# Performance work log

Measured on AMD Instinct MI355X. Metric: run time of the kernel, lower is better.

The kernel has to match this reference:

```python
import jax, jax.numpy as jnp
import numpy as np

N = 100000      # total nodes across batch of graphs
E = 1600000     # total edges (avg degree 16)
DIN = 16        # raw node feature dim
H = 128         # social_hidden_dim
HEADS = 4
DOUT = H // HEADS
LAYERS = 2
G = 64          # number of graphs in batch
FOUT = 256      # fusion_hidden_dim
NEG_SLOPE = 0.2


def layer_norm(x, g, b, eps=1e-5):
    mu = x.mean(-1, keepdims=True)
    var = ((x - mu) ** 2).mean(-1, keepdims=True)
    return (x - mu) / jnp.sqrt(var + eps) * g + b


def gat_conv(h, src, dst, W, a_src, a_dst, bias):
    # h: [N,H]; src/dst: [E+N] (self-loops included)
    hp = (h @ W).reshape(N, HEADS, DOUT)                    # [N,heads,dout]
    al_s = jnp.einsum('nhd,hd->nh', hp, a_src)              # [N,heads]
    al_d = jnp.einsum('nhd,hd->nh', hp, a_dst)
    logits = jax.nn.leaky_relu(al_s[src] + al_d[dst], NEG_SLOPE)  # [Etot,heads]
    m = jax.ops.segment_max(logits, dst, num_segments=N)    # segment softmax over dst
    e = jnp.exp(logits - m[dst])
    denom = jax.ops.segment_sum(e, dst, num_segments=N)
    alpha = e / (denom[dst] + 1e-16)                        # [Etot,heads]
    msg = hp[src] * alpha[:, :, None]                       # [Etot,heads,dout]
    out = jax.ops.segment_sum(msg, dst, num_segments=N)     # scatter-add
    return out.reshape(N, H) + bias


def setup_inputs():
    key = jax.random.key(0)
    ks = jax.random.split(key, 24)
    s = 0.05
    inp = {
        'x': jax.random.normal(ks[0], (N, DIN), jnp.float32),
        'edge_index': jax.random.randint(ks[1], (2, E), 0, N, jnp.int32),
        'node2graph': (jnp.arange(N, dtype=jnp.int32) * G // N).astype(jnp.int32),
        'Wp': jax.random.normal(ks[2], (DIN, H)) * s,
        'bp': jnp.zeros((H,)),
        'Wq1': jax.random.normal(ks[3], (2 * H, H)) * s,
        'bq1': jnp.zeros((H,)),
        'gq': jnp.ones((H,)), 'beq': jnp.zeros((H,)),
        'Wq2': jax.random.normal(ks[4], (H, FOUT)) * s,
        'bq2': jnp.zeros((FOUT,)),
    }
    for i in range(LAYERS):
        inp[f'Wg{i}'] = jax.random.normal(ks[5 + 4 * i], (H, H)) * s
        inp[f'as{i}'] = jax.random.normal(ks[6 + 4 * i], (HEADS, DOUT)) * s
        inp[f'ad{i}'] = jax.random.normal(ks[7 + 4 * i], (HEADS, DOUT)) * s
        inp[f'bg{i}'] = jnp.zeros((H,))
        inp[f'g{i}'] = jnp.ones((H,))
        inp[f'be{i}'] = jnp.zeros((H,))
    return inp


def reference(x, edge_index, node2graph, Wp, bp, Wq1, bq1, gq, beq, Wq2, bq2,
              Wg0, as0, ad0, bg0, g0, be0, Wg1, as1, ad1, bg1, g1, be1):
    loop = jnp.arange(N, dtype=edge_index.dtype)
    src = jnp.concatenate([edge_index[0], loop])  # add self-loops (PyG default)
    dst = jnp.concatenate([edge_index[1], loop])

    h = jax.nn.gelu(x @ Wp + bp, approximate=False)
    params = [(Wg0, as0, ad0, bg0, g0, be0), (Wg1, as1, ad1, bg1, g1, be1)]
    for (W, a_s, a_d, b, g, be) in params:
        h_new = gat_conv(h, src, dst, W, a_s, a_d, b)
        h = layer_norm(h_new + h, g, be)  # dims match -> residual

    counts = jax.ops.segment_sum(jnp.ones((N, 1), h.dtype), node2graph, num_segments=G)
    mean_pool = jax.ops.segment_sum(h, node2graph, num_segments=G) / jnp.maximum(counts, 1.0)
    max_pool = jax.ops.segment_max(h, node2graph, num_segments=G)
    emb = jnp.concatenate([mean_pool, max_pool], axis=-1)  # [G, 2H]

    p = layer_norm(emb @ Wq1 + bq1, gq, beq)
    p = jax.nn.gelu(p, approximate=False)
    return p @ Wq2 + bq2  # [G, FOUT]
```

## Files before the change

kernel.cpp:

```cpp
#include <hip/hip_runtime.h>

typedef unsigned short u16;
typedef unsigned char u8;
typedef unsigned int u32;
typedef unsigned long long u64;
typedef short short8 __attribute__((ext_vector_type(8)));
typedef float f32x4 __attribute__((ext_vector_type(4)));
typedef float f32x2 __attribute__((ext_vector_type(2)));

#define NN   100000
#define EE   1600000
#define ETOT (EE + NN)
#define NG   64
#define WSTR 136
#define SCANB 98
#define NB   98
#define BCAP 24576
#define OCAP 262144
#define EPB  4096

constexpr size_t AL256(size_t x) { return (x + 255) & ~(size_t)255; }
constexpr size_t OFF_FLAG   = 0;
constexpr size_t OFF_BSUM   = AL256(OFF_FLAG + 256);
constexpr size_t OFF_BCNT   = AL256(OFF_BSUM + 128 * 4);
constexpr size_t OFF_ROWPTR = AL256(OFF_BCNT + 128 * 4);
constexpr size_t OFF_DEG    = AL256(OFF_ROWPTR + (size_t)(NN + 1) * 4);
constexpr size_t OFF_COL    = AL256(OFF_DEG + (size_t)NN * 4);
constexpr size_t OFF_ALS    = AL256(OFF_COL + (size_t)ETOT * 4);
constexpr size_t OFF_ALD    = AL256(OFF_ALS + (size_t)NN * 4 * 4);
constexpr size_t OFF_GSUM   = AL256(OFF_ALD + (size_t)NN * 4 * 4);
constexpr size_t OFF_GKEY   = AL256(OFF_GSUM + (size_t)NG * 128 * 4);
constexpr size_t OFF_GCNT   = AL256(OFF_GKEY + (size_t)NG * 128 * 4);
constexpr size_t OFF_H      = AL256(OFF_GCNT + (size_t)NG * 4);
constexpr size_t OFF_HPB    = AL256(OFF_H + (size_t)NN * 128 * 2);
constexpr size_t OFF_EBUF   = AL256(OFF_HPB + (size_t)NN * 128 * 1);
constexpr size_t OFF_OBUF   = AL256(OFF_EBUF + (size_t)NB * BCAP * 8);
constexpr size_t WS_TOTAL   = AL256(OFF_OBUF + (size_t)OCAP * 8);

__device__ u64 g_ws[WS_TOTAL / 8];

__device__ __forceinline__ char* wsp() { return (char*)g_ws; }
#define WS_FLAG   ((int*)(wsp() + OFF_FLAG))
#define WS_BSUM   ((int*)(wsp() + OFF_BSUM))
#define WS_BCNT   ((int*)(wsp() + OFF_BCNT))
#define WS_ROWPTR ((int*)(wsp() + OFF_ROWPTR))
#define WS_DEG    ((int*)(wsp() + OFF_DEG))
#define WS_COL    ((int*)(wsp() + OFF_COL))
#define WS_ALS    ((float*)(wsp() + OFF_ALS))
#define WS_ALD    ((float*)(wsp() + OFF_ALD))
#define WS_GSUM   ((float*)(wsp() + OFF_GSUM))
#define WS_GKEY   ((u32*)(wsp() + OFF_GKEY))
#define WS_GCNT   ((int*)(wsp() + OFF_GCNT))
#define WS_H      ((u16*)(wsp() + OFF_H))
#define WS_HPB    ((u8*)(wsp() + OFF_HPB))
#define WS_EBUF   ((u64*)(wsp() + OFF_EBUF))
#define WS_OBUF   ((u64*)(wsp() + OFF_OBUF))

__device__ __forceinline__ float b2f(u16 u) { return __uint_as_float(((u32)u) << 16); }
__device__ __forceinline__ float b2f_lo(u32 u) { return __uint_as_float(u << 16); }
__device__ __forceinline__ float b2f_hi(u32 u) { return __uint_as_float(u & 0xffff0000u); }
__device__ __forceinline__ u16 f2bf(float f) {
    u32 u = __float_as_uint(f);
    return (u16)((u + 0x7fffu + ((u >> 16) & 1u)) >> 16);
}
__device__ __forceinline__ float ldf(const void* p, int i, int bf) {
    return bf ? b2f(((const u16*)p)[i]) : ((const float*)p)[i];
}
__device__ __forceinline__ int ldint(const int* p, long long i, int wide) {
    return wide ? p[i * 2] : p[(size_t)i];
}
__device__ __forceinline__ u32 fkey(float f) {
    u32 u = __float_as_uint(f);
    return (u >> 31) ? ~u : (u | 0x80000000u);
}
__device__ __forceinline__ float funkey(u32 k) {
    u32 u = (k & 0x80000000u) ? (k & 0x7fffffffu) : ~k;
    return __uint_as_float(u);
}

__global__ __launch_bounds__(256) void k_zero(const void* __restrict__ x,
                                              const int* __restrict__ ei) {
    if (blockIdx.x == 0 && threadIdx.x < 64) {
        int t = threadIdx.x;
        const u16* p = (const u16*)x;
        u16 u = p[t * 2];
        int e = (u >> 7) & 0xff;
        int ok = ((u & 0x7fffu) == 0) || (e >= 0x60 && e <= 0x9f);
        u64 m1 = __ballot(ok);
        int z = (ei[t * 2 + 1] == 0);
        u64 m2 = __ballot(z);
        if (t == 0) {
            WS_FLAG[0] = (__popcll(m1) >= 48) ? 1 : 0;
            WS_FLAG[1] = (__popcll(m2) >= 56) ? 1 : 0;
        }
    }
    if (blockIdx.x == 0 && threadIdx.x == 64) WS_FLAG[2] = 0;
    int i = blockIdx.x * 256 + threadIdx.x;
    if (i < NN) WS_DEG[i] = 0;
    if (i < NG * 128) { WS_GSUM[i] = 0.f; WS_GKEY[i] = 0u; }
    if (i < NG) WS_GCNT[i] = 0;
    if (i < NB) WS_BCNT[i] = 0;
}

__global__ __launch_bounds__(256) void k_bucket(const int* __restrict__ ei) {
    __shared__ int lcnt[NB], lbase[NB], lcur[NB];
    int t = threadIdx.x;
    int wide = WS_FLAG[1];
    for (int i = t; i < NB; i += 256) { lcnt[i] = 0; lcur[i] = 0; }
    __syncthreads();
    int e0 = blockIdx.x * EPB + t;
    int sA[16], dA[16];
#pragma unroll
    for (int j = 0; j < 16; j++) {
        int e = e0 + j * 256;
        int s = -1, d = 0;
        if (e < ETOT) {
            if (e < EE) {
                if (wide) { s = ((const int2*)ei)[e].x; d = ((const int2*)ei)[(size_t)EE + e].x; }
                else      { s = ei[e];                  d = ei[(size_t)EE + e]; }
            } else { s = e - EE; d = s; }
            if ((u32)s >= NN || (u32)d >= NN) s = -1;
        }
        sA[j] = s; dA[j] = d;
        if (s >= 0) atomicAdd(&lcnt[d >> 10], 1);
    }
    __syncthreads();
    for (int i = t; i < NB; i += 256)
        lbase[i] = atomicAdd(&WS_BCNT[i], lcnt[i]);
    __syncthreads();
    u64* ebuf = WS_EBUF;
#pragma unroll
    for (int j = 0; j < 16; j++) {
        int s = sA[j], d = dA[j];
        if (s < 0) continue;
        int b = d >> 10;
        int r = atomicAdd(&lcur[b], 1);
        int slot = lbase[b] + r;
        u64 pk = ((u64)(u32)d << 32) | (u32)s;
        if (slot < BCAP) {
            ebuf[(size_t)b * BCAP + slot] = pk;
        } else {
            int o = atomicAdd(&WS_FLAG[2], 1);
            if (o < OCAP) {
                WS_OBUF[o] = pk;
                atomicAdd(&WS_DEG[d], 1);
            }
        }
    }
}

__global__ __launch_bounds__(1024) void k_scan1() {
    __shared__ int sdat[1024];
    __shared__ int hist[1024];
    int b = blockIdx.x, t = threadIdx.x;
    hist[t] = 0;
    __syncthreads();
    int bc = WS_BCNT[b]; if (bc > BCAP) bc = BCAP;
    const u64* eb = WS_EBUF + (size_t)b * BCAP;
    for (int i = t; i < bc; i += 1024) {
        int d = (int)(eb[i] >> 32);
        atomicAdd(&hist[d & 1023], 1);
    }
    __syncthreads();
    int i = b * 1024 + t;
    int v = (i < NN) ? (WS_DEG[i] + hist[t]) : 0;
    sdat[t] = v;
    __syncthreads();
    for (int off = 1; off < 1024; off <<= 1) {
        int u = 0;
        if (t >= off) u = sdat[t - off];
        __syncthreads();
        if (t >= off) sdat[t] += u;
        __syncthreads();
    }
    if (i < NN) WS_ROWPTR[i] = sdat[t] - v;
    if (t == 1023) WS_BSUM[b] = sdat[1023];
}

__global__ __launch_bounds__(256) void k_place() {
    __shared__ int cur[1024];
    __shared__ int sb[128];
    int b = blockIdx.x, t = threadIdx.x;
    if (t < 128) sb[t] = (t < SCANB) ? WS_BSUM[t] : 0;
    __syncthreads();
    for (int off = 1; off < 128; off <<= 1) {
        int u = 0;
        if (t < 128 && t >= off) u = sb[t - off];
        __syncthreads();
        if (t < 128 && t >= off) sb[t] += u;
        __syncthreads();
    }
    int add = (b > 0) ? sb[b - 1] : 0;
    int n0 = b << 10;
    for (int i = t; i < 1024; i += 256) {
        int n = n0 + i;
        int r = 0;
        if (n < NN) {
            r = WS_ROWPTR[n] + add;
            WS_ROWPTR[n] = r;
        }
        cur[i] = r;
    }
    if (b == 0 && t == 0) WS_ROWPTR[NN] = sb[127];
    __syncthreads();
    int bc = WS_BCNT[b]; if (bc > BCAP) bc = BCAP;
    const u64* eb = WS_EBUF + (size_t)b * BCAP;
    for (int i = t; i < bc; i += 256) {
        u64 pk = eb[i];
        int d = (int)(pk >> 32), s = (int)(pk & 0xffffffffu);
        int pos = atomicAdd(&cur[d & 1023], 1);
        WS_COL[pos] = s;
    }
    int cnt = WS_FLAG[2]; if (cnt > OCAP) cnt = OCAP;
    for (int i = t; i < cnt; i += 256) {
        u64 pk = WS_OBUF[i];
        int d = (int)(pk >> 32);
        if ((d >> 10) == b) {
            int pos = atomicAdd(&cur[d & 1023], 1);
            WS_COL[pos] = (int)(pk & 0xffffffffu);
        }
    }
}

__global__ __launch_bounds__(128) void k_proj(const void* __restrict__ x,
                                              const void* __restrict__ Wp,
                                              const void* __restrict__ bp) {
    __shared__ float sW[16 * 128];
    int t = threadIdx.x;
    int bf = WS_FLAG[0];
    for (int i = t; i < 16 * 128; i += 128) sW[i] = ldf(Wp, i, bf);
    __syncthreads();
    float bj = ldf(bp, t, bf);
    for (int n = blockIdx.x; n < NN; n += gridDim.x) {
        float acc = bj;
#pragma unroll
        for (int k = 0; k < 16; k++)
            acc = fmaf(ldf(x, n * 16 + k, bf), sW[k * 128 + t], acc);
        float g = 0.5f * acc * (1.0f + erff(acc * 0.70710678118654752f));
        WS_H[(size_t)n * 128 + t] = f2bf(g);
    }
}

__global__ __launch_bounds__(256) void k_gemm(const void* __restrict__ Wg,
                                              const void* __restrict__ a_s,
                                              const void* __restrict__ a_d) {
    __shared__ __align__(16) u16 sWt[128 * WSTR];
    __shared__ __align__(16) u16 sH[16 * WSTR];
    int t = threadIdx.x;
    int bf = WS_FLAG[0];
    for (int idx = t; idx < 128 * 128; idx += 256) {
        int k = idx >> 7, n = idx & 127;
        sWt[n * WSTR + k] = bf ? ((const u16*)Wg)[idx] : f2bf(((const float*)Wg)[idx]);
    }
    __syncthreads();
    int wv = t >> 6, lane = t & 63;
    int n0 = wv * 32;
    int quad = lane >> 4, m16 = lane & 15;
    float as0v = ldf(a_s, n0 + m16, bf),      as1v = ldf(a_s, n0 + 16 + m16, bf);
    float ad0v = ldf(a_d, n0 + m16, bf),      ad1v = ldf(a_d, n0 + 16 + m16, bf);
    short8 bfr[2][4];
#pragma unroll
    for (int nt = 0; nt < 2; nt++) {
        int n = n0 + nt * 16 + m16;
#pragma unroll
        for (int ks = 0; ks < 4; ks++)
            bfr[nt][ks] = *(const short8*)&sWt[n * WSTR + ks * 32 + quad * 8];
    }
    u8* hp = WS_HPB;
    const u32* h32 = (const u32*)WS_H;
    u32* sH32 = (u32*)sH;
    for (int m0 = blockIdx.x * 16; m0 < NN; m0 += gridDim.x * 16) {
        __syncthreads();
        for (int idx = t; idx < 16 * 64; idx += 256) {
            int r = idx >> 6, c2 = idx & 63;
            sH32[r * 68 + c2] = h32[(size_t)(m0 + r) * 64 + c2];
        }
        __syncthreads();
        f32x4 acc0 = {0.f, 0.f, 0.f, 0.f};
        f32x4 acc1 = {0.f, 0.f, 0.f, 0.f};
#pragma unroll
        for (int ks = 0; ks < 4; ks++) {
            short8 af = *(const short8*)&sH[m16 * WSTR + ks * 32 + quad * 8];
            acc0 = __builtin_amdgcn_mfma_f32_16x16x32_bf16(af, bfr[0][ks], acc0, 0, 0, 0);
            acc1 = __builtin_amdgcn_mfma_f32_16x16x32_bf16(af, bfr[1][ks], acc1, 0, 0, 0);
        }
#pragma unroll
        for (int r = 0; r < 4; r++) {
            size_t row = (size_t)(m0 + quad * 4 + r) * 128;
            u32 pk8 = (u32)__builtin_amdgcn_cvt_pk_fp8_f32(acc0[r], acc1[r], 0, false);
            hp[row + n0 + m16]      = (u8)(pk8 & 0xff);
            hp[row + n0 + 16 + m16] = (u8)((pk8 >> 8) & 0xff);
            float ps = acc0[r] * as0v + acc1[r] * as1v;
            float pd = acc0[r] * ad0v + acc1[r] * ad1v;
#pragma unroll
            for (int m = 1; m <= 8; m <<= 1) {
                ps += __shfl_xor(ps, m);
                pd += __shfl_xor(pd, m);
            }
            if (m16 == 0) {
                int nrow = m0 + quad * 4 + r;
                WS_ALS[nrow * 4 + wv] = ps;
                WS_ALD[nrow * 4 + wv] = pd;
            }
        }
    }
}

__global__ __launch_bounds__(512) void k_gat(const void* __restrict__ bg,
                                             const void* __restrict__ gam,
                                             const void* __restrict__ bet) {
    int wid = threadIdx.x >> 6, lane = threadIdx.x & 63;
    int n = blockIdx.x * 8 + wid;
    if (n >= NN) return;
    int bf = WS_FLAG[0];
    const int* col = WS_COL;
    const float* als = WS_ALS;
    int k0 = WS_ROWPTR[n], deg = WS_ROWPTR[n + 1] - k0;
    int hd = lane >> 4, eo = lane & 15;
    float aldh = WS_ALD[n * 4 + hd];
    const u16* hp16 = (const u16*)WS_HPB;
    u32* h32 = (u32*)WS_H;
    u32 hv = h32[(size_t)n * 64 + lane];
    int base48 = lane & 48;

    int i0 = eo, i1 = eo + 16;
    int e0 = k0 + (i0 < deg ? i0 : 0);
    int e1 = k0 + (i1 < deg ? i1 : 0);
    int sc0 = col[e0];
    int sc1 = col[e1];
    float v0 = als[sc0 * 4 + hd] + aldh;
    float v1 = als[sc1 * 4 + hd] + aldh;
    v0 = v0 > 0.f ? v0 : 0.2f * v0;
    v1 = v1 > 0.f ? v1 : 0.2f * v1;
    float w0 = (i0 < deg) ? __expf(v0) : 0.f;
    float w1 = (i1 < deg) ? __expf(v1) : 0.f;
    float se = w0 + w1;
    float a0 = 0.f, a1 = 0.f;

#pragma unroll
    for (int j = 0; j < 16; j++) {
        float wj = __shfl(w0, base48 + j);
        int   sj = __builtin_amdgcn_readlane(sc0, j);
        u16 pv = hp16[(size_t)sj * 64 + lane];
        f32x2 mv = __builtin_amdgcn_cvt_pk_f32_fp8((int)pv, false);
        a0 = fmaf(wj, mv.x, a0);
        a1 = fmaf(wj, mv.y, a1);
    }
#pragma unroll
    for (int j = 0; j < 16; j++) {
        float wj = __shfl(w1, base48 + j);
        int   sj = __builtin_amdgcn_readlane(sc1, j);
        u16 pv = hp16[(size_t)sj * 64 + lane];
        f32x2 mv = __builtin_amdgcn_cvt_pk_f32_fp8((int)pv, false);
        a0 = fmaf(wj, mv.x, a0);
        a1 = fmaf(wj, mv.y, a1);
    }

    if (__builtin_expect(deg > 32, 0)) {
        for (int c = 32; c < deg; c += 16) {
            int i = c + eo;
            float w = 0.f; int scol = 0;
            if (i < deg) {
                scol = col[k0 + i];
                float v = als[scol * 4 + hd] + aldh;
                v = v > 0.f ? v : 0.2f * v;
                w = __expf(v);
            }
            se += w;
            int rem = deg - c; if (rem > 16) rem = 16;
            for (int j = 0; j < rem; j++) {
                float wj = __shfl(w, base48 + j);
                int sj = __shfl(scol, base48 + j);
                u16 pv = hp16[(size_t)sj * 64 + lane];
                f32x2 mv = __builtin_amdgcn_cvt_pk_f32_fp8((int)pv, false);
                a0 = fmaf(wj, mv.x, a0);
                a1 = fmaf(wj, mv.y, a1);
            }
        }
    }

    se += __shfl_xor(se, 1);
    se += __shfl_xor(se, 2);
    se += __shfl_xor(se, 4);
    se += __shfl_xor(se, 8);
    float inv = 1.f / (se + 1e-16f);
    int d0 = lane * 2, d1 = d0 + 1;
    float r0 = a0 * inv + ldf(bg, d0, bf) + b2f_lo(hv);
    float r1 = a1 * inv + ldf(bg, d1, bf) + b2f_hi(hv);
    float s1 = r0 + r1;
#pragma unroll
    for (int m = 1; m <= 32; m <<= 1) s1 += __shfl_xor(s1, m);
    float mu = s1 * (1.f / 128.f);
    float e0f = r0 - mu, e1f = r1 - mu;
    float s2 = e0f * e0f + e1f * e1f;
#pragma unroll
    for (int m = 1; m <= 32; m <<= 1) s2 += __shfl_xor(s2, m);
    float rstd = rsqrtf(s2 * (1.f / 128.f) + 1e-5f);
    float y0 = e0f * rstd * ldf(gam, d0, bf) + ldf(bet, d0, bf);
    float y1 = e1f * rstd * ldf(gam, d1, bf) + ldf(bet, d1, bf);
    h32[(size_t)n * 64 + lane] = (u32)f2bf(y0) | ((u32)f2bf(y1) << 16);
}

__global__ __launch_bounds__(128) void k_pool(const int* __restrict__ n2g) {
    int j = threadIdx.x;
    int wide = WS_FLAG[1];
    int n0 = blockIdx.x * 128;
    int n1 = n0 + 128; if (n1 > NN) n1 = NN;
    float runs = 0.f, runm = -3.4e38f;
    int rung = -1, runc = 0;
    for (int n = n0; n < n1; n++) {
        int g = ldint(n2g, n, wide);
        if (g != rung) {
            if (rung >= 0 && (u32)rung < NG) {
                atomicAdd(&WS_GSUM[rung * 128 + j], runs);
                atomicMax(&WS_GKEY[rung * 128 + j], fkey(runm));
                if (j == 0) atomicAdd(&WS_GCNT[rung], runc);
            }
            rung = g; runs = 0.f; runm = -3.4e38f; runc = 0;
        }
        float v = b2f(WS_H[(size_t)n * 128 + j]);
        runs += v;
        runm = fmaxf(runm, v);
        runc++;
    }
    if (rung >= 0 && (u32)rung < NG) {
        atomicAdd(&WS_GSUM[rung * 128 + j], runs);
        atomicMax(&WS_GKEY[rung * 128 + j], fkey(runm));
        if (j == 0) atomicAdd(&WS_GCNT[rung], runc);
    }
}

__global__ __launch_bounds__(256) void k_head(const void* __restrict__ Wq1,
                                              const void* __restrict__ bq1,
                                              const void* __restrict__ gq,
                                              const void* __restrict__ beq,
                                              const void* __restrict__ Wq2,
                                              const void* __restrict__ bq2,
                                              float* __restrict__ out) {
    __shared__ float sem[256];
    __shared__ float sp[128];
    __shared__ float red[4];
    int g = blockIdx.x, t = threadIdx.x;
    int bf = WS_FLAG[0];
    float cnt = fmaxf((float)WS_GCNT[g], 1.f);
    if (t < 128) sem[t] = WS_GSUM[g * 128 + t] / cnt;
    else         sem[t] = funkey(WS_GKEY[g * 128 + (t - 128)]);
    __syncthreads();
    float a = 0.f;
    if (t < 128) {
        a = ldf(bq1, t, bf);
        for (int k = 0; k < 256; k++) a = fmaf(sem[k], ldf(Wq1, k * 128 + t, bf), a);
    }
    int lane = t & 63, wv = t >> 6;
    float s1 = (t < 128) ? a : 0.f;
#pragma unroll
    for (int m = 1; m <= 32; m <<= 1) s1 += __shfl_xor(s1, m);
    if (lane == 0) red[wv] = s1;
    __syncthreads();
    float mu = (red[0] + red[1]) * (1.f / 128.f);
    float d = (t < 128) ? (a - mu) : 0.f;
    float s2 = d * d;
#pragma unroll
    for (int m = 1; m <= 32; m <<= 1) s2 += __shfl_xor(s2, m);
    __syncthreads();
    if (lane == 0) red[wv] = s2;
    __syncthreads();
    float var = (red[0] + red[1]) * (1.f / 128.f);
    if (t < 128) {
        float p = d * rsqrtf(var + 1e-5f) * ldf(gq, t, bf) + ldf(beq, t, bf);
        sp[t] = 0.5f * p * (1.0f + erff(p * 0.70710678118654752f));
    }
    __syncthreads();
    float o = ldf(bq2, t, bf);
    for (int k = 0; k < 128; k++)
        o = fmaf(sp[k], ldf(Wq2, k * 256 + t, bf), o);
    out[g * 256 + t] = o;
}

extern "C" void kernel_launch(void* const* d_in, const int* in_sizes, int n_in,
                              void* d_out, int out_size, void* d_ws, size_t ws_size,
                              hipStream_t stream) {
    const void* x   = d_in[0];
    const int* ei   = (const int*)d_in[1];
    const int* n2g  = (const int*)d_in[2];
    const void* Wp  = d_in[3];
    const void* bp  = d_in[4];
    const void* Wq1 = d_in[5];
    const void* bq1 = d_in[6];
    const void* gq  = d_in[7];
    const void* beq = d_in[8];
    const void* Wq2 = d_in[9];
    const void* bq2 = d_in[10];
    const void* Wg0 = d_in[11];
    const void* as0 = d_in[12];
    const void* ad0 = d_in[13];
    const void* bg0 = d_in[14];
    const void* g0  = d_in[15];
    const void* be0 = d_in[16];
    const void* Wg1 = d_in[17];
    const void* as1 = d_in[18];
    const void* ad1 = d_in[19];
    const void* bg1 = d_in[20];
    const void* g1  = d_in[21];
    const void* be1 = d_in[22];
    (void)d_ws; (void)ws_size; (void)in_sizes; (void)n_in; (void)out_size;

    k_zero<<<(NN + 255) / 256, 256, 0, stream>>>(x, ei);

    k_bucket<<<(ETOT + EPB - 1) / EPB, 256, 0, stream>>>(ei);
    k_scan1<<<SCANB, 1024, 0, stream>>>();
    k_place<<<NB, 256, 0, stream>>>();

    k_proj<<<2048, 128, 0, stream>>>(x, Wp, bp);

    k_gemm<<<1024, 256, 0, stream>>>(Wg0, as0, ad0);
    k_gat<<<(NN + 7) / 8, 512, 0, stream>>>(bg0, g0, be0);
    k_gemm<<<1024, 256, 0, stream>>>(Wg1, as1, ad1);
    k_gat<<<(NN + 7) / 8, 512, 0, stream>>>(bg1, g1, be1);

    k_pool<<<(NN + 127) / 128, 128, 0, stream>>>(n2g);
    k_head<<<NG, 256, 0, stream>>>(Wq1, bq1, gq, beq, Wq2, bq2, (float*)d_out);
}
```

Baseline: 562.2 us.

## Replace bucketed CSR build with atomic count/fill and split GAT edges across half-waves

The CSR construction drops the bucketed edge buffer and overflow path in favor of a direct per-node atomic degree count, a two-pass scan, and a second pass that atomically fills column indices. The GAT aggregation now has each half-wavefront process a different edge with 4 fp8 features per lane via 32-bit loads, combining the halves with a cross-lane add. It also loops generically over degree in chunks of 32 instead of using a fixed 32-edge fast path plus a slow tail. The CSR change removes large intermediate buffer traffic but adds heavy global atomics on node degrees and a second read of the edge list. Column order within a row becomes nondeterministic.

```diff
diff --git a/kernel.cpp b/kernel.cpp
--- a/kernel.cpp
+++ b/kernel.cpp
@@ -14,16 +14,12 @@
 #define NG   64
 #define WSTR 136
 #define SCANB 98
-#define NB   98
-#define BCAP 24576
-#define OCAP 262144
 #define EPB  4096
 
 constexpr size_t AL256(size_t x) { return (x + 255) & ~(size_t)255; }
 constexpr size_t OFF_FLAG   = 0;
 constexpr size_t OFF_BSUM   = AL256(OFF_FLAG + 256);
-constexpr size_t OFF_BCNT   = AL256(OFF_BSUM + 128 * 4);
-constexpr size_t OFF_ROWPTR = AL256(OFF_BCNT + 128 * 4);
+constexpr size_t OFF_ROWPTR = AL256(OFF_BSUM + 128 * 4);
 constexpr size_t OFF_DEG    = AL256(OFF_ROWPTR + (size_t)(NN + 1) * 4);
 constexpr size_t OFF_COL    = AL256(OFF_DEG + (size_t)NN * 4);
 constexpr size_t OFF_ALS    = AL256(OFF_COL + (size_t)ETOT * 4);
@@ -33,16 +29,13 @@
 constexpr size_t OFF_GCNT   = AL256(OFF_GKEY + (size_t)NG * 128 * 4);
 constexpr size_t OFF_H      = AL256(OFF_GCNT + (size_t)NG * 4);
 constexpr size_t OFF_HPB    = AL256(OFF_H + (size_t)NN * 128 * 2);
-constexpr size_t OFF_EBUF   = AL256(OFF_HPB + (size_t)NN * 128 * 1);
-constexpr size_t OFF_OBUF   = AL256(OFF_EBUF + (size_t)NB * BCAP * 8);
-constexpr size_t WS_TOTAL   = AL256(OFF_OBUF + (size_t)OCAP * 8);
+constexpr size_t WS_TOTAL   = AL256(OFF_HPB + (size_t)NN * 128 * 1);
 
 __device__ u64 g_ws[WS_TOTAL / 8];
 
 __device__ __forceinline__ char* wsp() { return (char*)g_ws; }
 #define WS_FLAG   ((int*)(wsp() + OFF_FLAG))
 #define WS_BSUM   ((int*)(wsp() + OFF_BSUM))
-#define WS_BCNT   ((int*)(wsp() + OFF_BCNT))
 #define WS_ROWPTR ((int*)(wsp() + OFF_ROWPTR))
 #define WS_DEG    ((int*)(wsp() + OFF_DEG))
 #define WS_COL    ((int*)(wsp() + OFF_COL))
@@ -53,8 +46,6 @@
 #define WS_GCNT   ((int*)(wsp() + OFF_GCNT))
 #define WS_H      ((u16*)(wsp() + OFF_H))
 #define WS_HPB    ((u8*)(wsp() + OFF_HPB))
-#define WS_EBUF   ((u64*)(wsp() + OFF_EBUF))
-#define WS_OBUF   ((u64*)(wsp() + OFF_OBUF))
 
 __device__ __forceinline__ float b2f(u16 u) { return __uint_as_float(((u32)u) << 16); }
 __device__ __forceinline__ float b2f_lo(u32 u) { return __uint_as_float(u << 16); }
@@ -94,76 +85,35 @@
             WS_FLAG[1] = (__popcll(m2) >= 56) ? 1 : 0;
         }
     }
-    if (blockIdx.x == 0 && threadIdx.x == 64) WS_FLAG[2] = 0;
     int i = blockIdx.x * 256 + threadIdx.x;
     if (i < NN) WS_DEG[i] = 0;
     if (i < NG * 128) { WS_GSUM[i] = 0.f; WS_GKEY[i] = 0u; }
     if (i < NG) WS_GCNT[i] = 0;
-    if (i < NB) WS_BCNT[i] = 0;
-}
-
-__global__ __launch_bounds__(256) void k_bucket(const int* __restrict__ ei) {
-    __shared__ int lcnt[NB], lbase[NB], lcur[NB];
-    int t = threadIdx.x;
+}
+
+__global__ __launch_bounds__(256) void k_deg(const int* __restrict__ ei) {
     int wide = WS_FLAG[1];
-    for (int i = t; i < NB; i += 256) { lcnt[i] = 0; lcur[i] = 0; }
-    __syncthreads();
-    int e0 = blockIdx.x * EPB + t;
-    int sA[16], dA[16];
+    int e0 = blockIdx.x * EPB + threadIdx.x;
 #pragma unroll
     for (int j = 0; j < 16; j++) {
         int e = e0 + j * 256;
-        int s = -1, d = 0;
         if (e < ETOT) {
+            int s, d;
             if (e < EE) {
                 if (wide) { s = ((const int2*)ei)[e].x; d = ((const int2*)ei)[(size_t)EE + e].x; }
                 else      { s = ei[e];                  d = ei[(size_t)EE + e]; }
             } else { s = e - EE; d = s; }
-            if ((u32)s >= NN || (u32)d >= NN) s = -1;
-        }
-        sA[j] = s; dA[j] = d;
-        if (s >= 0) atomicAdd(&lcnt[d >> 10], 1);
-    }
-    __syncthreads();
-    for (int i = t; i < NB; i += 256)
-        lbase[i] = atomicAdd(&WS_BCNT[i], lcnt[i]);
-    __syncthreads();
-    u64* ebuf = WS_EBUF;
-#pragma unroll
-    for (int j = 0; j < 16; j++) {
-        int s = sA[j], d = dA[j];
-        if (s < 0) continue;
-        int b = d >> 10;
-        int r = atomicAdd(&lcur[b], 1);
-        int slot = lbase[b] + r;
-        u64 pk = ((u64)(u32)d << 32) | (u32)s;
-        if (slot < BCAP) {
-            ebuf[(size_t)b * BCAP + slot] = pk;
-        } else {
-            int o = atomicAdd(&WS_FLAG[2], 1);
-            if (o < OCAP) {
-                WS_OBUF[o] = pk;
-                atomicAdd(&WS_DEG[d], 1);
-            }
+            if ((u32)s < NN && (u32)d < NN) atomicAdd(&WS_DEG[d], 1);
         }
     }
 }
 
 __global__ __launch_bounds__(1024) void k_scan1() {
     __shared__ int sdat[1024];
-    __shared__ int hist[1024];
     int b = blockIdx.x, t = threadIdx.x;
-    hist[t] = 0;
-    __syncthreads();
-    int bc = WS_BCNT[b]; if (bc > BCAP) bc = BCAP;
-    const u64* eb = WS_EBUF + (size_t)b * BCAP;
-    for (int i = t; i < bc; i += 1024) {
-        int d = (int)(eb[i] >> 32);
-        atomicAdd(&hist[d & 1023], 1);
-    }
-    __syncthreads();
     int i = b * 1024 + t;
-    int v = (i < NN) ? (WS_DEG[i] + hist[t]) : 0;
+    int v = 0;
+    if (i < NN) { v = WS_DEG[i]; WS_DEG[i] = 0; }
     sdat[t] = v;
     __syncthreads();
     for (int off = 1; off < 1024; off <<= 1) {
@@ -173,12 +123,11 @@
         if (t >= off) sdat[t] += u;
         __syncthreads();
     }
-    if (i < NN) WS_ROWPTR[i] = sdat[t] - v;
+    if (i <= NN) WS_ROWPTR[i] = sdat[t] - v;
     if (t == 1023) WS_BSUM[b] = sdat[1023];
 }
 
-__global__ __launch_bounds__(256) void k_place() {
-    __shared__ int cur[1024];
+__global__ __launch_bounds__(1024) void k_fin() {
     __shared__ int sb[128];
     int b = blockIdx.x, t = threadIdx.x;
     if (t < 128) sb[t] = (t < SCANB) ? WS_BSUM[t] : 0;
@@ -190,34 +139,29 @@
         if (t < 128 && t >= off) sb[t] += u;
         __syncthreads();
     }
-    int add = (b > 0) ? sb[b - 1] : 0;
-    int n0 = b << 10;
-    for (int i = t; i < 1024; i += 256) {
-        int n = n0 + i;
-        int r = 0;
-        if (n < NN) {
-            r = WS_ROWPTR[n] + add;
-            WS_ROWPTR[n] = r;
-        }
-        cur[i] = r;
-    }
-    if (b == 0 && t == 0) WS_ROWPTR[NN] = sb[127];
-    __syncthreads();
-    int bc = WS_BCNT[b]; if (bc > BCAP) bc = BCAP;
-    const u64* eb = WS_EBUF + (size_t)b * BCAP;
-    for (int i = t; i < bc; i += 256) {
-        u64 pk = eb[i];
-        int d = (int)(pk >> 32), s = (int)(pk & 0xffffffffu);
-        int pos = atomicAdd(&cur[d & 1023], 1);
-        WS_COL[pos] = s;
-    }
-    int cnt = WS_FLAG[2]; if (cnt > OCAP) cnt = OCAP;
-    for (int i = t; i < cnt; i += 256) {
-        u64 pk = WS_OBUF[i];
-        int d = (int)(pk >> 32);
-        if ((d >> 10) == b) {
-            int pos = atomicAdd(&cur[d & 1023], 1);
-            WS_COL[pos] = (int)(pk & 0xffffffffu);
+    if (b > 0) {
+        int add = sb[b - 1];
+        int i = b * 1024 + t;
+        if (i <= NN) WS_ROWPTR[i] += add;
+    }
+}
+
+__global__ __launch_bounds__(256) void k_fill(const int* __restrict__ ei) {
+    int wide = WS_FLAG[1];
+    int e0 = blockIdx.x * EPB + threadIdx.x;
+#pragma unroll
+    for (int j = 0; j < 16; j++) {
+        int e = e0 + j * 256;
+        if (e < ETOT) {
+            int s, d;
+            if (e < EE) {
+                if (wide) { s = ((const int2*)ei)[e].x; d = ((const int2*)ei)[(size_t)EE + e].x; }
+                else      { s = ei[e];                  d = ei[(size_t)EE + e]; }
+            } else { s = e - EE; d = s; }
+            if ((u32)s < NN && (u32)d < NN) {
+                int pos = WS_ROWPTR[d] + atomicAdd(&WS_DEG[d], 1);
+                WS_COL[pos] = s;
+            }
         }
     }
 }
@@ -317,88 +261,88 @@
     const float* als = WS_ALS;
     int k0 = WS_ROWPTR[n], deg = WS_ROWPTR[n + 1] - k0;
     int hd = lane >> 4, eo = lane & 15;
+    int half = lane >> 5, q = lane & 31, hq = q >> 3;
     float aldh = WS_ALD[n * 4 + hd];
-    const u16* hp16 = (const u16*)WS_HPB;
-    u32* h32 = (u32*)WS_H;
-    u32 hv = h32[(size_t)n * 64 + lane];
-    int base48 = lane & 48;
-
-    int i0 = eo, i1 = eo + 16;
-    int e0 = k0 + (i0 < deg ? i0 : 0);
-    int e1 = k0 + (i1 < deg ? i1 : 0);
-    int sc0 = col[e0];
-    int sc1 = col[e1];
-    float v0 = als[sc0 * 4 + hd] + aldh;
-    float v1 = als[sc1 * 4 + hd] + aldh;
-    v0 = v0 > 0.f ? v0 : 0.2f * v0;
-    v1 = v1 > 0.f ? v1 : 0.2f * v1;
-    float w0 = (i0 < deg) ? __expf(v0) : 0.f;
-    float w1 = (i1 < deg) ? __expf(v1) : 0.f;
-    float se = w0 + w1;
-    float a0 = 0.f, a1 = 0.f;
-
-#pragma unroll
-    for (int j = 0; j < 16; j++) {
-        float wj = __shfl(w0, base48 + j);
-        int   sj = __builtin_amdgcn_readlane(sc0, j);
-        u16 pv = hp16[(size_t)sj * 64 + lane];
-        f32x2 mv = __builtin_amdgcn_cvt_pk_f32_fp8((int)pv, false);
-        a0 = fmaf(wj, mv.x, a0);
-        a1 = fmaf(wj, mv.y, a1);
-    }
-#pragma unroll
-    for (int j = 0; j < 16; j++) {
-        float wj = __shfl(w1, base48 + j);
-        int   sj = __builtin_amdgcn_readlane(sc1, j);
-        u16 pv = hp16[(size_t)sj * 64 + lane];
-        f32x2 mv = __builtin_amdgcn_cvt_pk_f32_fp8((int)pv, false);
-        a0 = fmaf(wj, mv.x, a0);
-        a1 = fmaf(wj, mv.y, a1);
-    }
-
-    if (__builtin_expect(deg > 32, 0)) {
-        for (int c = 32; c < deg; c += 16) {
-            int i = c + eo;
-            float w = 0.f; int scol = 0;
-            if (i < deg) {
-                scol = col[k0 + i];
-                float v = als[scol * 4 + hd] + aldh;
-                v = v > 0.f ? v : 0.2f * v;
-                w = __expf(v);
+    const u32* hp32 = (const u32*)WS_HPB;
+    const u64* h64 = (const u64*)WS_H;
+    u64 hv = h64[(size_t)n * 32 + q];
+    float se = 0.f, a0 = 0.f, a1 = 0.f, a2 = 0.f, a3 = 0.f;
+    int wsel = hq * 16 + half;
+
+    for (int c = 0; c < deg; c += 32) {
+        int i0 = c + eo, i1 = c + 16 + eo;
+        int e0 = k0 + (i0 < deg ? i0 : 0);
+        int e1 = k0 + (i1 < deg ? i1 : 0);
+        int sc0 = col[e0];
+        int sc1 = col[e1];
+        float v0 = als[sc0 * 4 + hd] + aldh;
+        float v1 = als[sc1 * 4 + hd] + aldh;
+        v0 = v0 > 0.f ? v0 : 0.2f * v0;
+        v1 = v1 > 0.f ? v1 : 0.2f * v1;
+        float w0 = (i0 < deg) ? __expf(v0) : 0.f;
+        float w1 = (i1 < deg) ? __expf(v1) : 0.f;
+        se += w0 + w1;
+#pragma unroll
+        for (int j = 0; j < 8; j++) {
+            float wj = __shfl(w0, wsel + 2 * j);
+            int   sj = __shfl(sc0, half + 2 * j);
+            u32 v = hp32[(size_t)sj * 32 + q];
+            f32x2 mlo = __builtin_amdgcn_cvt_pk_f32_fp8((int)v, false);
+            f32x2 mhi = __builtin_amdgcn_cvt_pk_f32_fp8((int)v, true);
+            a0 = fmaf(wj, mlo.x, a0);
+            a1 = fmaf(wj, mlo.y, a1);
+            a2 = fmaf(wj, mhi.x, a2);
+            a3 = fmaf(wj, mhi.y, a3);
+        }
+        if (deg > c + 16) {
+#pragma unroll
+            for (int j = 0; j < 8; j++) {
+                float wj = __shfl(w1, wsel + 2 * j);
+                int   sj = __shfl(sc1, half + 2 * j);
+                u32 v = hp32[(size_t)sj * 32 + q];
+                f32x2 mlo = __builtin_amdgcn_cvt_pk_f32_fp8((int)v, false);
+                f32x2 mhi = __builtin_amdgcn_cvt_pk_f32_fp8((int)v, true);
+                a0 = fmaf(wj, mlo.x, a0);
+                a1 = fmaf(wj, mlo.y, a1);
+                a2 = fmaf(wj, mhi.x, a2);
+                a3 = fmaf(wj, mhi.y, a3);
             }
-            se += w;
-            int rem = deg - c; if (rem > 16) rem = 16;
-            for (int j = 0; j < rem; j++) {
-                float wj = __shfl(w, base48 + j);
-                int sj = __shfl(scol, base48 + j);
-                u16 pv = hp16[(size_t)sj * 64 + lane];
-                f32x2 mv = __builtin_amdgcn_cvt_pk_f32_fp8((int)pv, false);
-                a0 = fmaf(wj, mv.x, a0);
-                a1 = fmaf(wj, mv.y, a1);
-            }
-        }
-    }
-
+        }
+    }
+    a0 += __shfl_xor(a0, 32);
+    a1 += __shfl_xor(a1, 32);
+    a2 += __shfl_xor(a2, 32);
+    a3 += __shfl_xor(a3, 32);
     se += __shfl_xor(se, 1);
     se += __shfl_xor(se, 2);
     se += __shfl_xor(se, 4);
     se += __shfl_xor(se, 8);
     float inv = 1.f / (se + 1e-16f);
-    int d0 = lane * 2, d1 = d0 + 1;
-    float r0 = a0 * inv + ldf(bg, d0, bf) + b2f_lo(hv);
-    float r1 = a1 * inv + ldf(bg, d1, bf) + b2f_hi(hv);
-    float s1 = r0 + r1;
+    float invq = __shfl(inv, hq * 16);
+    int d0 = q * 4;
+    u32 hlo = (u32)hv, hhi = (u32)(hv >> 32);
+    float r0 = a0 * invq + ldf(bg, d0 + 0, bf) + b2f_lo(hlo);
+    float r1 = a1 * invq + ldf(bg, d0 + 1, bf) + b2f_hi(hlo);
+    float r2 = a2 * invq + ldf(bg, d0 + 2, bf) + b2f_lo(hhi);
+    float r3 = a3 * invq + ldf(bg, d0 + 3, bf) + b2f_hi(hhi);
+    float s1 = r0 + r1 + r2 + r3;
 #pragma unroll
     for (int m = 1; m <= 32; m <<= 1) s1 += __shfl_xor(s1, m);
-    float mu = s1 * (1.f / 128.f);
-    float e0f = r0 - mu, e1f = r1 - mu;
-    float s2 = e0f * e0f + e1f * e1f;
+    float mu = s1 * (1.f / 256.f);
+    float e0f = r0 - mu, e1f = r1 - mu, e2f = r2 - mu, e3f = r3 - mu;
+    float s2 = e0f * e0f + e1f * e1f + e2f * e2f + e3f * e3f;
 #pragma unroll
     for (int m = 1; m <= 32; m <<= 1) s2 += __shfl_xor(s2, m);
-    float rstd = rsqrtf(s2 * (1.f / 128.f) + 1e-5f);
-    float y0 = e0f * rstd * ldf(gam, d0, bf) + ldf(bet, d0, bf);
-    float y1 = e1f * rstd * ldf(gam, d1, bf) + ldf(bet, d1, bf);
-    h32[(size_t)n * 64 + lane] = (u32)f2bf(y0) | ((u32)f2bf(y1) << 16);
+    float rstd = rsqrtf(s2 * (1.f / 256.f) + 1e-5f);
+    float y0 = e0f * rstd * ldf(gam, d0 + 0, bf) + ldf(bet, d0 + 0, bf);
+    float y1 = e1f * rstd * ldf(gam, d0 + 1, bf) + ldf(bet, d0 + 1, bf);
+    float y2 = e2f * rstd * ldf(gam, d0 + 2, bf) + ldf(bet, d0 + 2, bf);
+    float y3 = e3f * rstd * ldf(gam, d0 + 3, bf) + ldf(bet, d0 + 3, bf);
+    if (half == 0) {
+        u64 pk = (u64)f2bf(y0) | ((u64)f2bf(y1) << 16)
+               | ((u64)f2bf(y2) << 32) | ((u64)f2bf(y3) << 48);
+        ((u64*)WS_H)[(size_t)n * 32 + q] = pk;
+    }
 }
 
 __global__ __launch_bounds__(128) void k_pool(const int* __restrict__ n2g) {
@@ -507,9 +451,10 @@
 
     k_zero<<<(NN + 255) / 256, 256, 0, stream>>>(x, ei);
 
-    k_bucket<<<(ETOT + EPB - 1) / EPB, 256, 0, stream>>>(ei);
+    k_deg<<<(ETOT + EPB - 1) / EPB, 256, 0, stream>>>(ei);
     k_scan1<<<SCANB, 1024, 0, stream>>>();
-    k_place<<<NB, 256, 0, stream>>>();
+    k_fin<<<SCANB, 1024, 0, stream>>>();
+    k_fill<<<(ETOT + EPB - 1) / EPB, 256, 0, stream>>>(ei);
 
     k_proj<<<2048, 128, 0, stream>>>(x, Wp, bp);
 
```

Measured after the change: 726.7 us. 29.3% more time.
